# Kernel optimization log

Hardware: AMD Instinct MI355X
Metric: run time of the kernel (lower is better)

## Reference

```python
import jax, jax.numpy as jnp
import numpy as np

E = 80000   # number of directed edges
T = 80000   # number of triplets
HID = 256   # hidden_channels
INT = 64    # int_emb_size == num_bilinear
NR = 6      # num_radial
NS = 7      # num_spherical
BD = 8      # basis_emb_size_dist
BA = 8      # basis_emb_size_angle


def swish(x):
    return x * jax.nn.sigmoid(x)


def setup_inputs() -> dict:
    key = jax.random.key(0)
    ks = jax.random.split(key, 16)
    inp = {
        "x1": jax.random.normal(ks[0], (E, HID), dtype=jnp.float32),
        "rbf0": jax.random.normal(ks[1], (E, NR), dtype=jnp.float32),
        "sbf": jax.random.normal(ks[2], (T, NS * NR), dtype=jnp.float32),
        "t": jax.random.normal(ks[3], (T, NS * NS * NR), dtype=jnp.float32),
        "x_kj": jax.random.normal(ks[4], (E, HID), dtype=jnp.float32),
        "x_ji": jax.random.normal(ks[5], (E, HID), dtype=jnp.float32),
        "idx_kj": jax.random.randint(ks[6], (T,), 0, E, dtype=jnp.int32),
        "idx_ji": jax.random.randint(ks[7], (T,), 0, E, dtype=jnp.int32),
        # weights stored [in, out] so y = x @ W (torch Linear uses weight.T)
        "W_rbf1": jax.random.normal(ks[8], (NR, BD), dtype=jnp.float32) * 0.3,
        "W_rbf2": jax.random.normal(ks[9], (BD, HID), dtype=jnp.float32) * 0.3,
        "W_sbf1": jax.random.normal(ks[10], (NS * NR, BA), dtype=jnp.float32) * 0.15,
        "W_sbf2": jax.random.normal(ks[11], (BA, INT), dtype=jnp.float32) * 0.3,
        "W_t1": jax.random.normal(ks[12], (NS * NS * NR, INT), dtype=jnp.float32) * 0.06,
        "W_down": jax.random.normal(ks[13], (HID, INT), dtype=jnp.float32) * 0.06,
        "W_up": jax.random.normal(ks[14], (INT, HID), dtype=jnp.float32) * 0.12,
        # bilinear weight W: [int_emb, num_bilinear, int_emb], std = 2/int_emb
        "W_bil": jax.random.normal(ks[15], (INT, INT, INT), dtype=jnp.float32) * (2.0 / INT),
    }
    return inp


def reference(x1, rbf0, sbf, t, x_kj, x_ji, idx_kj, idx_ji,
              W_rbf1, W_rbf2, W_sbf1, W_sbf2, W_t1, W_down, W_up, W_bil):
    # rbf projection: [E, NR] -> [E, HID]
    rbf = (rbf0 @ W_rbf1) @ W_rbf2
    xk = x_kj * rbf                          # [E, HID]
    xk = swish(xk @ W_down)                  # [E, INT]
    # sbf projection: [T, NS*NR] -> [T, INT]
    s = (sbf @ W_sbf1) @ W_sbf2
    xk = xk[idx_kj] * s                      # gather to triplets: [T, INT]
    tt = t @ W_t1                            # [T, INT] (num_bilinear dim)
    # bilinear: 'wj,wl,ijl->wi' with W_bil [INT(i), INT(j), INT(l)]
    a = jnp.einsum('wj,ijl->wil', tt, W_bil)  # [T, INT, INT]
    out_t = jnp.einsum('wil,wl->wi', a, xk)   # [T, INT]
    # scatter-add triplets back to edges
    agg = jax.ops.segment_sum(out_t, idx_ji, num_segments=x1.shape[0])  # [E, INT]
    return swish(agg @ W_up)                  # [E, HID]
```

## Files before the change

kernel.cpp:

```cpp
#include <hip/hip_runtime.h>
#include <hip/hip_fp16.h>

#define E_N 80000
#define T_N 80000

typedef _Float16 h4 __attribute__((ext_vector_type(4)));
typedef _Float16 h8 __attribute__((ext_vector_type(8)));
typedef float    f4 __attribute__((ext_vector_type(4)));
typedef float    f2 __attribute__((ext_vector_type(2)));
typedef unsigned int u4 __attribute__((ext_vector_type(4)));

static __device__ __forceinline__ float swishf(float x) {
    return x / (1.0f + __expf(-x));
}

static __device__ __forceinline__ void pack_w_dev(const float* __restrict__ src,
                                                  h8* __restrict__ dst,
                                                  int g, int Ksrc, int N, int NT) {
    int lane = g & 63, frag = g >> 6;
    int nt = frag % NT, kt = frag / NT;
    int quad = (lane >> 4);
    int n = nt * 16 + (lane & 15);
    int k0 = kt * 32 + quad * 8;
    h8 v;
#pragma unroll
    for (int u = 0; u < 8; ++u) {
        int k = k0 + u;
        v[u] = (k < Ksrc) ? (_Float16)src[(size_t)k * N + n] : (_Float16)0.0f;
    }
    dst[g] = v;
}

__global__ __launch_bounds__(256) void kpack_all(const float* __restrict__ Wb,  h8* __restrict__ wbil,
                                                 const float* __restrict__ Wd,  h8* __restrict__ wpd,
                                                 const float* __restrict__ Wt,  h8* __restrict__ wpt,
                                                 const float* __restrict__ Wu,  h8* __restrict__ wpu) {
    int b = blockIdx.x, tid = threadIdx.x;
    if (b < 128) {
        int g = b * 256 + tid;
        int i    = ((g >> 6) & 3) * 16 + (g & 15);
        int c    = (g >> 8) & 1;
        int j    = g >> 9;
        int quad = (g >> 4) & 3;
        int l0   = c * 32 + quad * 8;
        const float* src = Wb + ((i * 64 + j) << 6) + l0;
        h8 v;
#pragma unroll
        for (int u = 0; u < 8; ++u) v[u] = (_Float16)src[u];
        wbil[g] = v;
    } else if (b < 136) {
        pack_w_dev(Wd, wpd, (b - 128) * 256 + tid, 256, 64, 4);
    } else if (b < 146) {
        pack_w_dev(Wt, wpt, (b - 136) * 256 + tid, 294, 64, 4);
    } else {
        pack_w_dev(Wu, wpu, (b - 146) * 256 + tid, 64, 256, 16);
    }
}

__global__ __launch_bounds__(256, 4) void k1_down(const float* __restrict__ rbf0,
                                                  const float* __restrict__ xkj,
                                                  const float* __restrict__ W_rbf1,
                                                  const float* __restrict__ W_rbf2,
                                                  const h8* __restrict__ wpd,
                                                  _Float16* __restrict__ xke) {
    int tid = threadIdx.x;
    int lane = tid & 63, wv = tid >> 6;
    int m = lane & 15, quad = lane >> 4;
    int rowb = blockIdx.x * 128 + wv * 32;

    float r8[2][8];
#pragma unroll
    for (int rt = 0; rt < 2; ++rt) {
        int r = rowb + rt * 16 + m;
        float rv[6];
#pragma unroll
        for (int q = 0; q < 6; ++q) rv[q] = rbf0[(size_t)r * 6 + q];
#pragma unroll
        for (int p = 0; p < 8; ++p) {
            float s = 0.f;
#pragma unroll
            for (int q = 0; q < 6; ++q) s += rv[q] * W_rbf1[q * 8 + p];
            r8[rt][p] = s;
        }
    }

    f4 acc[2][4] = {};
#pragma unroll
    for (int kb = 0; kb < 8; ++kb) {
        int k0 = kb * 32 + quad * 8;
        h8 afrag[2];
#pragma unroll
        for (int rt = 0; rt < 2; ++rt) {
            f4 rlo = {}, rhi = {};
#pragma unroll
            for (int p = 0; p < 8; ++p) {
                rlo += r8[rt][p] * *(const f4*)(W_rbf2 + p * 256 + k0);
                rhi += r8[rt][p] * *(const f4*)(W_rbf2 + p * 256 + k0 + 4);
            }
            size_t base = (size_t)(rowb + rt * 16 + m) * 256 + k0;
            f4 xlo = *(const f4*)(xkj + base);
            f4 xhi = *(const f4*)(xkj + base + 4);
            rlo *= xlo; rhi *= xhi;
            h8 a;
#pragma unroll
            for (int u = 0; u < 4; ++u) {
                a[u]     = (_Float16)rlo[u];
                a[u + 4] = (_Float16)rhi[u];
            }
            afrag[rt] = a;
        }
#pragma unroll
        for (int nt = 0; nt < 4; ++nt) {
            h8 b = wpd[((kb * 4 + nt) << 6) + lane];
            acc[0][nt] = __builtin_amdgcn_mfma_f32_16x16x32_f16(afrag[0], b, acc[0][nt], 0, 0, 0);
            acc[1][nt] = __builtin_amdgcn_mfma_f32_16x16x32_f16(afrag[1], b, acc[1][nt], 0, 0, 0);
        }
    }

#pragma unroll
    for (int rt = 0; rt < 2; ++rt)
#pragma unroll
        for (int nt = 0; nt < 4; ++nt)
#pragma unroll
            for (int rr = 0; rr < 4; ++rr) {
                int row = rowb + rt * 16 + quad * 4 + rr;
                xke[(size_t)row * 64 + nt * 16 + m] = (_Float16)swishf(acc[rt][nt][rr]);
            }
}

__global__ __launch_bounds__(256) void kb1_tproj(const float* __restrict__ tin,
                                                 const h8* __restrict__ wpt,
                                                 _Float16* __restrict__ ttb) {
    int tid = threadIdx.x;
    int lane = tid & 63, wv = tid >> 6;
    int m = lane & 15, quad = lane >> 4;
    int rowb = blockIdx.x * 128 + wv * 32;

    f4 acc[2][4] = {};
    for (int ktg = 0; ktg < 10; ++ktg) {
        int k0 = ktg * 32 + quad * 8;
        h8 afrag[2];
#pragma unroll
        for (int rt = 0; rt < 2; ++rt) {
            size_t base = (size_t)(rowb + rt * 16 + m) * 294 + k0;
            h8 a;
            if (k0 + 8 <= 294) {
                f2 t0 = *(const f2*)(tin + base);
                f2 t1 = *(const f2*)(tin + base + 2);
                f2 t2 = *(const f2*)(tin + base + 4);
                f2 t3 = *(const f2*)(tin + base + 6);
                a[0] = (_Float16)t0[0]; a[1] = (_Float16)t0[1];
                a[2] = (_Float16)t1[0]; a[3] = (_Float16)t1[1];
                a[4] = (_Float16)t2[0]; a[5] = (_Float16)t2[1];
                a[6] = (_Float16)t3[0]; a[7] = (_Float16)t3[1];
            } else {
#pragma unroll
                for (int u = 0; u < 8; ++u) {
                    int k = k0 + u;
                    a[u] = (k < 294) ? (_Float16)tin[base + u] : (_Float16)0.0f;
                }
            }
            afrag[rt] = a;
        }
#pragma unroll
        for (int nt = 0; nt < 4; ++nt) {
            h8 b = wpt[((ktg * 4 + nt) << 6) + lane];
#pragma unroll
            for (int rt = 0; rt < 2; ++rt)
                acc[rt][nt] = __builtin_amdgcn_mfma_f32_16x16x32_f16(afrag[rt], b, acc[rt][nt], 0, 0, 0);
        }
    }

#pragma unroll
    for (int rt = 0; rt < 2; ++rt)
#pragma unroll
        for (int nt = 0; nt < 4; ++nt)
#pragma unroll
            for (int rr = 0; rr < 4; ++rr) {
                int row = rowb + rt * 16 + quad * 4 + rr;
                ttb[(size_t)row * 64 + nt * 16 + m] = (_Float16)acc[rt][nt][rr];
            }
}

__global__ __launch_bounds__(256) void kb2_gather(const float* __restrict__ sbf,
                                                  const float* __restrict__ W_sbf1,
                                                  const float* __restrict__ W_sbf2,
                                                  const _Float16* __restrict__ xke,
                                                  const int* __restrict__ idx_kj,
                                                  _Float16* __restrict__ xkt) {
    __shared__ float sbfL[32 * 42];
    __shared__ float midL[32 * 8];
    int tid = threadIdx.x;
    int row0 = blockIdx.x * 32;
    for (int i = tid; i < 32 * 42; i += 256)
        sbfL[i] = sbf[(size_t)row0 * 42 + i];
    __syncthreads();
    {
        int r = tid >> 3, p = tid & 7;
        float mm = 0.f;
#pragma unroll
        for (int q = 0; q < 42; ++q) mm += sbfL[r * 42 + q] * W_sbf1[q * 8 + p];
        midL[r * 8 + p] = mm;
    }
    __syncthreads();
    int r = tid >> 3;
    int c0 = (tid & 7) * 8;
    int w = row0 + r;
    int e = idx_kj[w];
    f4 sa = {}, sb = {};
#pragma unroll
    for (int p = 0; p < 8; ++p) {
        float mm = midL[r * 8 + p];
        sa += mm * *(const f4*)(W_sbf2 + (p << 6) + c0);
        sb += mm * *(const f4*)(W_sbf2 + (p << 6) + c0 + 4);
    }
    h8 xv = *(const h8*)(xke + (size_t)e * 64 + c0);
    h8 o;
#pragma unroll
    for (int u = 0; u < 4; ++u) {
        o[u]     = (_Float16)((float)xv[u]     * sa[u]);
        o[u + 4] = (_Float16)((float)xv[u + 4] * sb[u]);
    }
    *(h8*)(xkt + (size_t)w * 64 + c0) = o;
}

__global__ __launch_bounds__(128, 3) void kb3_bilinear(const _Float16* __restrict__ xkt,
                                                       const _Float16* __restrict__ ttp,
                                                       const h8* __restrict__ wpack,
                                                       const int* __restrict__ idx_ji,
                                                       float* __restrict__ agg) {
    int tid = threadIdx.x;
    int lane = tid & 63, wv = tid >> 6;
    int qrow = lane & 15, quad = lane >> 4;
    int row0 = blockIdx.x * 128 + wv * 64;
    int jlo = blockIdx.y * 32;

    h8 xa[4][2];
#pragma unroll
    for (int rt = 0; rt < 4; ++rt) {
        const _Float16* rp = xkt + (size_t)(row0 + rt * 16 + qrow) * 64 + quad * 8;
        xa[rt][0] = *(const h8*)rp;
        xa[rt][1] = *(const h8*)(rp + 32);
    }

    f4 acc[4][4] = {};
#pragma unroll
    for (int jg = 0; jg < 4; ++jg) {
        h8 tg[4];
#pragma unroll
        for (int rt = 0; rt < 4; ++rt)
            tg[rt] = *(const h8*)(ttp + (size_t)(row0 + rt * 16 + qrow) * 64 + jlo + jg * 8);
#pragma unroll
        for (int ju = 0; ju < 8; ++ju) {
            int j = jlo + jg * 8 + ju;
            const h8* wj = wpack + (((size_t)j * 8) << 6) + lane;
            h8 b0[4], b1[4];
#pragma unroll
            for (int nt = 0; nt < 4; ++nt) {
                b0[nt] = wj[nt << 6];
                b1[nt] = wj[(4 + nt) << 6];
            }
#pragma unroll
            for (int rt = 0; rt < 4; ++rt) {
                _Float16 tv = tg[rt][ju];
                h8 t8 = {tv, tv, tv, tv, tv, tv, tv, tv};
                h8 a0 = xa[rt][0] * t8;
                h8 a1 = xa[rt][1] * t8;
#pragma unroll
                for (int nt = 0; nt < 4; ++nt) {
                    acc[rt][nt] = __builtin_amdgcn_mfma_f32_16x16x32_f16(a0, b0[nt], acc[rt][nt], 0, 0, 0);
                    acc[rt][nt] = __builtin_amdgcn_mfma_f32_16x16x32_f16(a1, b1[nt], acc[rt][nt], 0, 0, 0);
                }
            }
        }
    }

#pragma unroll
    for (int rt = 0; rt < 4; ++rt) {
#pragma unroll
        for (int rr = 0; rr < 4; ++rr) {
            int w = row0 + rt * 16 + quad * 4 + rr;
            int e = idx_ji[w];
            float* dst = agg + (size_t)e * 64 + qrow;
#pragma unroll
            for (int nt = 0; nt < 4; ++nt)
                atomicAdd(dst + nt * 16, acc[rt][nt][rr]);
        }
    }
}

__global__ __launch_bounds__(256) void k4_up(const float* __restrict__ agg,
                                             const h8* __restrict__ wpu,
                                             float* __restrict__ out) {
    int tid = threadIdx.x;
    int lane = tid & 63, wv = tid >> 6;
    int m = lane & 15, quad = lane >> 4;
    int rowb = blockIdx.x * 64 + wv * 16;

    f4 acc[16] = {};
#pragma unroll
    for (int kt = 0; kt < 2; ++kt) {
        const float* ap = agg + (size_t)(rowb + m) * 64 + kt * 32 + quad * 8;
        f4 alo = *(const f4*)ap;
        f4 ahi = *(const f4*)(ap + 4);
        h8 a;
#pragma unroll
        for (int u = 0; u < 4; ++u) {
            a[u]     = (_Float16)alo[u];
            a[u + 4] = (_Float16)ahi[u];
        }
#pragma unroll
        for (int nt = 0; nt < 16; ++nt) {
            h8 b = wpu[((kt * 16 + nt) << 6) + lane];
            acc[nt] = __builtin_amdgcn_mfma_f32_16x16x32_f16(a, b, acc[nt], 0, 0, 0);
        }
    }

#pragma unroll
    for (int nt = 0; nt < 16; ++nt)
#pragma unroll
        for (int rr = 0; rr < 4; ++rr) {
            int row = rowb + quad * 4 + rr;
            out[(size_t)row * 256 + nt * 16 + m] = swishf(acc[nt][rr]);
        }
}

extern "C" void kernel_launch(void* const* d_in, const int* in_sizes, int n_in,
                              void* d_out, int out_size, void* d_ws, size_t ws_size,
                              hipStream_t stream) {
    const float* rbf0   = (const float*)d_in[1];
    const float* sbf    = (const float*)d_in[2];
    const float* tin    = (const float*)d_in[3];
    const float* xkj    = (const float*)d_in[4];
    const int*   idx_kj = (const int*)d_in[6];
    const int*   idx_ji = (const int*)d_in[7];
    const float* W_rbf1 = (const float*)d_in[8];
    const float* W_rbf2 = (const float*)d_in[9];
    const float* W_sbf1 = (const float*)d_in[10];
    const float* W_sbf2 = (const float*)d_in[11];
    const float* W_t1   = (const float*)d_in[12];
    const float* W_down = (const float*)d_in[13];
    const float* W_up   = (const float*)d_in[14];
    const float* W_bil  = (const float*)d_in[15];

    char* ws = (char*)d_ws;
    _Float16* xke = (_Float16*)ws;
    float*    agg = (float*)(ws + 10240000);
    h8* wpack_bil = (h8*)(ws + 30720000);
    h8* wpd       = (h8*)(ws + 31244288);
    h8* wpt       = (h8*)(ws + 31277056);
    h8* wpu       = (h8*)(ws + 31318016);
    _Float16* ttb = (_Float16*)d_out;
    _Float16* xkt = (_Float16*)((char*)d_out + 10240000);
    float*    out = (float*)d_out;

    hipMemsetAsync(agg, 0, (size_t)E_N * 64 * 4, stream);
    kpack_all<<<154, 256, 0, stream>>>(W_bil, wpack_bil, W_down, wpd, W_t1, wpt, W_up, wpu);
    k1_down<<<625, 256, 0, stream>>>(rbf0, xkj, W_rbf1, W_rbf2, wpd, xke);
    kb1_tproj<<<625, 256, 0, stream>>>(tin, wpt, ttb);
    kb2_gather<<<2500, 256, 0, stream>>>(sbf, W_sbf1, W_sbf2, xke, idx_kj, xkt);
    kb3_bilinear<<<dim3(625, 2), 128, 0, stream>>>(xkt, ttb, wpack_bil, idx_ji, agg);
    k4_up<<<1250, 256, 0, stream>>>(agg, wpu, out);
}
```

Baseline: 474.7 us.

## Replace atomic scatter-add with counting-sort CSR and segmented reduction

Builds a per-edge histogram of idx_ji inside the gather kernel, then runs a three-pass prefix scan and a fill pass to give each triplet a slot in an edge-sorted order. The bilinear kernel now writes its results to those slots with plain stores, one buffer per column half, instead of doing float atomicAdds into agg. A new kagg kernel sums each edge's contiguous range. This removes contended random float atomics and the memset of agg. In exchange it adds several small kernel launches and an extra write and read of about 41 MB of triplet partials.

```diff
diff --git a/kernel.cpp b/kernel.cpp
--- a/kernel.cpp
+++ b/kernel.cpp
@@ -3,12 +3,12 @@
 
 #define E_N 80000
 #define T_N 80000
+#define NB1 313
 
 typedef _Float16 h4 __attribute__((ext_vector_type(4)));
 typedef _Float16 h8 __attribute__((ext_vector_type(8)));
 typedef float    f4 __attribute__((ext_vector_type(4)));
 typedef float    f2 __attribute__((ext_vector_type(2)));
-typedef unsigned int u4 __attribute__((ext_vector_type(4)));
 
 static __device__ __forceinline__ float swishf(float x) {
     return x / (1.0f + __expf(-x));
@@ -187,11 +187,14 @@
                                                   const float* __restrict__ W_sbf2,
                                                   const _Float16* __restrict__ xke,
                                                   const int* __restrict__ idx_kj,
+                                                  const int* __restrict__ idx_ji,
+                                                  int* __restrict__ hist,
                                                   _Float16* __restrict__ xkt) {
     __shared__ float sbfL[32 * 42];
     __shared__ float midL[32 * 8];
     int tid = threadIdx.x;
     int row0 = blockIdx.x * 32;
+    if (tid < 32) atomicAdd(&hist[idx_ji[row0 + tid]], 1);
     for (int i = tid; i < 32 * 42; i += 256)
         sbfL[i] = sbf[(size_t)row0 * 42 + i];
     __syncthreads();
@@ -224,11 +227,65 @@
     *(h8*)(xkt + (size_t)w * 64 + c0) = o;
 }
 
+__global__ __launch_bounds__(256) void kscan1(const int* __restrict__ hist, int* __restrict__ bsum) {
+    int t = threadIdx.x;
+    int w = blockIdx.x * 256 + t;
+    int v = (w < E_N) ? hist[w] : 0;
+#pragma unroll
+    for (int off = 32; off; off >>= 1) v += __shfl_down(v, off, 64);
+    __shared__ int ls[4];
+    if ((t & 63) == 0) ls[t >> 6] = v;
+    __syncthreads();
+    if (t == 0) bsum[blockIdx.x] = ls[0] + ls[1] + ls[2] + ls[3];
+}
+
+__global__ __launch_bounds__(512) void kscan2(const int* __restrict__ bsum, int* __restrict__ boff) {
+    __shared__ int s[512];
+    int t = threadIdx.x;
+    int v = (t < NB1) ? bsum[t] : 0;
+    s[t] = v;
+    __syncthreads();
+    for (int off = 1; off < 512; off <<= 1) {
+        int x = (t >= off) ? s[t - off] : 0;
+        __syncthreads();
+        s[t] += x;
+        __syncthreads();
+    }
+    if (t < NB1) boff[t] = s[t] - v;
+}
+
+__global__ __launch_bounds__(256) void kscan3(const int* __restrict__ hist, const int* __restrict__ boff,
+                                              int* __restrict__ start, int* __restrict__ nxt) {
+    __shared__ int s[256];
+    int t = threadIdx.x;
+    int w = blockIdx.x * 256 + t;
+    int v = (w < E_N) ? hist[w] : 0;
+    s[t] = v;
+    __syncthreads();
+    for (int off = 1; off < 256; off <<= 1) {
+        int x = (t >= off) ? s[t - off] : 0;
+        __syncthreads();
+        s[t] += x;
+        __syncthreads();
+    }
+    if (w < E_N) {
+        int st = boff[blockIdx.x] + s[t] - v;
+        start[w] = st;
+        nxt[w]   = st;
+    }
+}
+
+__global__ __launch_bounds__(256) void kfill(const int* __restrict__ idx_ji,
+                                             int* __restrict__ nxt, int* __restrict__ pos) {
+    int w = blockIdx.x * 256 + threadIdx.x;
+    if (w < T_N) pos[w] = atomicAdd(&nxt[idx_ji[w]], 1);
+}
+
 __global__ __launch_bounds__(128, 3) void kb3_bilinear(const _Float16* __restrict__ xkt,
                                                        const _Float16* __restrict__ ttp,
                                                        const h8* __restrict__ wpack,
-                                                       const int* __restrict__ idx_ji,
-                                                       float* __restrict__ agg) {
+                                                       const int* __restrict__ pos,
+                                                       float* __restrict__ outp) {
     int tid = threadIdx.x;
     int lane = tid & 63, wv = tid >> 6;
     int qrow = lane & 15, quad = lane >> 4;
@@ -275,18 +332,35 @@
         }
     }
 
+    float* __restrict__ outh = outp + (size_t)blockIdx.y * ((size_t)T_N * 64);
 #pragma unroll
     for (int rt = 0; rt < 4; ++rt) {
 #pragma unroll
         for (int rr = 0; rr < 4; ++rr) {
             int w = row0 + rt * 16 + quad * 4 + rr;
-            int e = idx_ji[w];
-            float* dst = agg + (size_t)e * 64 + qrow;
+            float* dst = outh + (size_t)pos[w] * 64 + qrow;
 #pragma unroll
             for (int nt = 0; nt < 4; ++nt)
-                atomicAdd(dst + nt * 16, acc[rt][nt][rr]);
-        }
-    }
+                dst[nt * 16] = acc[rt][nt][rr];
+        }
+    }
+}
+
+__global__ __launch_bounds__(256) void kagg(const float* __restrict__ outp,
+                                            const int* __restrict__ start,
+                                            const int* __restrict__ nxt,
+                                            float* __restrict__ agg) {
+    int tid = threadIdx.x;
+    int e = blockIdx.x * 16 + (tid >> 4);
+    int c4 = (tid & 15) * 4;
+    int p0 = start[e], p1 = nxt[e];
+    const float* o1 = outp + (size_t)T_N * 64;
+    f4 s = {0.f, 0.f, 0.f, 0.f};
+    for (int p = p0; p < p1; ++p) {
+        s += *(const f4*)(outp + (size_t)p * 64 + c4);
+        s += *(const f4*)(o1   + (size_t)p * 64 + c4);
+    }
+    *(f4*)(agg + (size_t)e * 64 + c4) = s;
 }
 
 __global__ __launch_bounds__(256) void k4_up(const float* __restrict__ agg,
@@ -350,15 +424,29 @@
     h8* wpd       = (h8*)(ws + 31244288);
     h8* wpt       = (h8*)(ws + 31277056);
     h8* wpu       = (h8*)(ws + 31318016);
-    _Float16* ttb = (_Float16*)d_out;
-    _Float16* xkt = (_Float16*)((char*)d_out + 10240000);
-    float*    out = (float*)d_out;
-
-    hipMemsetAsync(agg, 0, (size_t)E_N * 64 * 4, stream);
+
+    char* ob = (char*)d_out;
+    _Float16* ttb  = (_Float16*)ob;
+    _Float16* xkt  = (_Float16*)(ob + 10240000);
+    float*    outp = (float*)(ob + 20480000);
+    int* hist  = (int*)(ob + 61440000);
+    int* start = (int*)(ob + 61760000);
+    int* nxt   = (int*)(ob + 62080000);
+    int* pos   = (int*)(ob + 62400000);
+    int* bsum  = (int*)(ob + 62720000);
+    int* boff  = (int*)(ob + 62724096);
+    float* out = (float*)d_out;
+
+    hipMemsetAsync(hist, 0, E_N * 4, stream);
     kpack_all<<<154, 256, 0, stream>>>(W_bil, wpack_bil, W_down, wpd, W_t1, wpt, W_up, wpu);
     k1_down<<<625, 256, 0, stream>>>(rbf0, xkj, W_rbf1, W_rbf2, wpd, xke);
     kb1_tproj<<<625, 256, 0, stream>>>(tin, wpt, ttb);
-    kb2_gather<<<2500, 256, 0, stream>>>(sbf, W_sbf1, W_sbf2, xke, idx_kj, xkt);
-    kb3_bilinear<<<dim3(625, 2), 128, 0, stream>>>(xkt, ttb, wpack_bil, idx_ji, agg);
+    kb2_gather<<<2500, 256, 0, stream>>>(sbf, W_sbf1, W_sbf2, xke, idx_kj, idx_ji, hist, xkt);
+    kscan1<<<NB1, 256, 0, stream>>>(hist, bsum);
+    kscan2<<<1, 512, 0, stream>>>(bsum, boff);
+    kscan3<<<NB1, 256, 0, stream>>>(hist, boff, start, nxt);
+    kfill<<<NB1, 256, 0, stream>>>(idx_ji, nxt, pos);
+    kb3_bilinear<<<dim3(625, 2), 128, 0, stream>>>(xkt, ttb, wpack_bil, pos, outp);
+    kagg<<<5000, 256, 0, stream>>>(outp, start, nxt, agg);
     k4_up<<<1250, 256, 0, stream>>>(agg, wpu, out);
 }
```

Measured after the change: 474.6 us. No clear change (-0.0%).
